# Kernel tuning notes

Hardware: AMD Instinct MI355X
Metric: run time of the kernel (lower is better)

## Reference

```python
import jax, jax.numpy as jnp
import numpy as np

B, T, H_DIM, N_HEADS, FACTOR = 1, 2048, 2048, 16, 2
KEY_DIM = H_DIM // N_HEADS          # 128
V_DIM = H_DIM * FACTOR              # 4096
HEAD_DIM = V_DIM // N_HEADS         # 256
SCALING = KEY_DIM ** -0.5
EPS = 1e-6


def rotate_every_two(x):
    x1 = x[..., ::2]
    x2 = x[..., 1::2]
    return jnp.stack([-x2, x1], axis=-1).reshape(x.shape)


def theta_shift(x, sin, cos):
    return x * cos + rotate_every_two(x) * sin


def setup_inputs() -> dict:
    key = jax.random.key(0)
    ks = jax.random.split(key, 11)
    s = 0.02  # xavier-ish init scale
    inp = {
        'hidden_states': jax.random.normal(ks[0], (B, T, H_DIM), jnp.float32),
        'Wq': jax.random.normal(ks[1], (H_DIM, H_DIM), jnp.float32) * s,
        'bq': jnp.zeros((H_DIM,), jnp.float32),
        'Wk': jax.random.normal(ks[2], (H_DIM, H_DIM), jnp.float32) * s,
        'bk': jnp.zeros((H_DIM,), jnp.float32),
        'Wv': jax.random.normal(ks[3], (H_DIM, V_DIM), jnp.float32) * s,
        'bv': jnp.zeros((V_DIM,), jnp.float32),
        'Wg': jax.random.normal(ks[4], (H_DIM, V_DIM), jnp.float32) * s,
        'bg': jnp.zeros((V_DIM,), jnp.float32),
        'Wo': jax.random.normal(ks[5], (V_DIM, H_DIM), jnp.float32) * s,
        'bo': jnp.zeros((H_DIM,), jnp.float32),
    }
    # --- RetNetRelPos (parallel mode), as in syncdoth/RetNet ---
    angle = 1.0 / (10000 ** np.linspace(0, 1, KEY_DIM // 2))
    angle = np.repeat(angle, 2)                      # [key_dim]
    index = np.arange(T)
    inp['sin'] = jnp.asarray(np.sin(index[:, None] * angle[None, :]).astype(np.float32))
    inp['cos'] = jnp.asarray(np.cos(index[:, None] * angle[None, :]).astype(np.float32))
    decay = np.log(1 - 2.0 ** (-5 - np.arange(N_HEADS, dtype=np.float64)))  # [h], negative
    diff = index[:, None] - index[None, :]           # [T,T]
    tri = diff >= 0                                  # causal mask
    expo = decay[:, None, None] * np.where(tri, diff, 0)[None]  # [h,T,T]
    mask = np.where(tri[None], np.exp(expo), 0.0)
    mask = mask / np.sqrt(mask.sum(-1, keepdims=True))
    inp['decay_mask'] = jnp.asarray(mask[None].astype(np.float32))  # [1,h,T,T]
    return inp


def _msr_forward(hidden_states, sin, cos, decay_mask,
                 Wq, bq, Wk, bk, Wv, bv, Wg, bg, Wo, bo):
    Bsz, Tlen, _ = hidden_states.shape
    q = hidden_states @ Wq + bq                      # [B,T,H]
    k = hidden_states @ Wk + bk
    v = hidden_states @ Wv + bv                      # [B,T,V_DIM]
    g = hidden_states @ Wg + bg
    # split heads -> [B,h,T,dim]
    q = q.reshape(Bsz, Tlen, N_HEADS, KEY_DIM).transpose(0, 2, 1, 3)
    k = k.reshape(Bsz, Tlen, N_HEADS, KEY_DIM).transpose(0, 2, 1, 3)
    v = v.reshape(Bsz, Tlen, N_HEADS, HEAD_DIM).transpose(0, 2, 1, 3)
    k = k * SCALING
    qr = theta_shift(q, sin, cos)                    # sin/cos broadcast over B,h
    kr = theta_shift(k, sin, cos)
    # parallel retention: QK^T scaled by decay mask, row-normalized (detached denom)
    retention = jnp.einsum('bhsk,bhtk->bhst', qr, kr) * decay_mask
    denom = jnp.clip(jnp.abs(jax.lax.stop_gradient(retention).sum(-1, keepdims=True)), 1.0, None)
    retention = retention / denom
    out = jnp.einsum('bhst,bhtd->bshd', retention, v)  # [B,T,h,head_dim]
    # group_norm: LayerNorm over head_dim, eps=1e-6, no affine
    mu = out.mean(-1, keepdims=True)
    var = out.var(-1, keepdims=True)
    normed = ((out - mu) / jnp.sqrt(var + EPS)).reshape(Bsz, Tlen, V_DIM)
    gated = jax.nn.silu(g) * normed
    return gated @ Wo + bo                           # [B,T,H]


def reference(hidden_states, sin, cos, decay_mask,
              Wq, bq, Wk, bk, Wv, bv, Wg, bg, Wo, bo):
    return _msr_forward(hidden_states, sin, cos, decay_mask,
                        Wq, bq, Wk, bk, Wv, bv, Wg, bg, Wo, bo)
```

## Files before the change

### kernel.cpp

```cpp
#include <hip/hip_runtime.h>
#include <hip/hip_bf16.h>

typedef __hip_bfloat16 bf16;
typedef __attribute__((ext_vector_type(8))) __bf16 bf16x8;
typedef __attribute__((ext_vector_type(4))) float f32x4;

constexpr int TT = 2048;
constexpr int HD = 2048;
constexpr int VD = 4096;
constexpr int KD = 128;
constexpr int NH = 16;
constexpr int DH = 256;
constexpr float K_SCALING = 0.08838834764831845f;

__device__ __forceinline__ bf16 f2bf(float x) { return __float2bfloat16(x); }
__device__ __forceinline__ unsigned short f2bfu(float x) {
    bf16 b = __float2bfloat16(x);
    return *reinterpret_cast<unsigned short*>(&b);
}
__device__ __forceinline__ float bf2f(unsigned short u) {
    unsigned int x = ((unsigned int)u) << 16;
    return __uint_as_float(x);
}

__global__ __launch_bounds__(256) void transpose_all_k(
    const float* __restrict__ Wq, const float* __restrict__ Wk,
    const float* __restrict__ Wv, const float* __restrict__ Wg,
    const float* __restrict__ Wo, bf16* __restrict__ Wcat, bf16* __restrict__ WoT,
    const float* __restrict__ hidden, bf16* __restrict__ hb)
{
    __shared__ unsigned short sT[64 * 72];
    int t2 = blockIdx.x;
    if (t2 >= 8192) {
        const int b = t2 - 8192;
        const size_t base = (size_t)b * 8192;
#pragma unroll
        for (int j = 0; j < 8; ++j) {
            const size_t i = base + j * 1024 + threadIdx.x * 4;
            float4 v = *(const float4*)(hidden + i);
            bf16 tmp[4] = {f2bf(v.x), f2bf(v.y), f2bf(v.z), f2bf(v.w)};
            *(uint2*)(hb + i) = *(const uint2*)tmp;
        }
        return;
    }
    const float* src;
    bf16* dst;
    int R, C;
    if (t2 < 1024)      { src = Wq; dst = Wcat;                     R = 2048; C = 2048; }
    else if (t2 < 2048) { src = Wk; dst = Wcat + (size_t)2048 * HD; R = 2048; C = 2048; t2 -= 1024; }
    else if (t2 < 4096) { src = Wv; dst = Wcat + (size_t)4096 * HD; R = 2048; C = 4096; t2 -= 2048; }
    else if (t2 < 6144) { src = Wg; dst = Wcat + (size_t)8192 * HD; R = 2048; C = 4096; t2 -= 4096; }
    else                { src = Wo; dst = WoT;                      R = 4096; C = 2048; t2 -= 6144; }
    const int xt = C >> 6;
    const int x0 = (t2 % xt) * 64;
    const int y0 = (t2 / xt) * 64;

    const int t = threadIdx.x;
    {
        const int r = t >> 2;
        const int c0 = (t & 3) << 4;
        const float* s = src + (size_t)(y0 + r) * C + x0 + c0;
        unsigned short e[16];
#pragma unroll
        for (int j = 0; j < 4; ++j) {
            float4 v = *(const float4*)(s + j * 4);
            e[j * 4 + 0] = f2bfu(v.x);
            e[j * 4 + 1] = f2bfu(v.y);
            e[j * 4 + 2] = f2bfu(v.z);
            e[j * 4 + 3] = f2bfu(v.w);
        }
#pragma unroll
        for (int i = 0; i < 16; ++i) {
            const int c = c0 + i;
            sT[c * 72 + (r ^ (((c >> 3) & 7) << 3))] = e[i];
        }
    }
    __syncthreads();
    {
        const int c = t >> 2;
        const int r0 = (t & 3) << 4;
        const int xs = ((c >> 3) & 7) << 3;
#pragma unroll
        for (int s2 = 0; s2 < 16; s2 += 8) {
            bf16x8 v = *(const bf16x8*)&sT[c * 72 + ((r0 + s2) ^ xs)];
            *(bf16x8*)&dst[(size_t)(x0 + c) * R + y0 + r0 + s2] = v;
        }
    }
}

__global__ __launch_bounds__(256) void transpose_bf16_k(const bf16* __restrict__ in,
                                                        bf16* __restrict__ outb) {
    __shared__ unsigned short sT[64 * 72];
    const int tid = threadIdx.x;
    const int x0 = blockIdx.x * 64;
    const int y0 = blockIdx.y * 64;
    {
        const int lt = tid >> 2;
        const int c0 = (tid & 3) << 4;
        unsigned short e[16];
        *(bf16x8*)&e[0] = *(const bf16x8*)&in[(size_t)(y0 + lt) * VD + x0 + c0];
        *(bf16x8*)&e[8] = *(const bf16x8*)&in[(size_t)(y0 + lt) * VD + x0 + c0 + 8];
#pragma unroll
        for (int i = 0; i < 16; ++i) {
            const int c = c0 + i;
            sT[c * 72 + (lt ^ (((c >> 3) & 7) << 3))] = e[i];
        }
    }
    __syncthreads();
    {
        const int c = tid >> 2;
        const int r0 = (tid & 3) << 4;
        const int xs = ((c >> 3) & 7) << 3;
#pragma unroll
        for (int s2 = 0; s2 < 16; s2 += 8) {
            bf16x8 v = *(const bf16x8*)&sT[c * 72 + ((r0 + s2) ^ xs)];
            *(bf16x8*)&outb[(size_t)(x0 + c) * TT + y0 + r0 + s2] = v;
        }
    }
}

#define GLL(gptr, lptr) __builtin_amdgcn_global_load_lds( \
    (const __attribute__((address_space(1))) void*)(gptr), \
    (__attribute__((address_space(3))) void*)(lptr), 16, 0, 0)

#define STA(bufs, u, k1) GLL(gA0 + (size_t)((u) * 64) * HD + (k1), sA + (bufs) + (u) * 4096 + tid * 8)
#define STB(bufs, u, k1) GLL(gB0 + (size_t)((u) * 64) * HD + (k1), sB + (bufs) + (u) * 4096 + tid * 8)

#define WAIT6 asm volatile("s_waitcnt vmcnt(6)" ::: "memory")
#define WAIT0V asm volatile("s_waitcnt vmcnt(0)" ::: "memory")
#define MEMF asm volatile("" ::: "memory")
#define BAR __builtin_amdgcn_s_barrier()

#define LDA(dst, cb, qm) \
    _Pragma("unroll") for (int mi = 0; mi < 4; ++mi) { \
        const int r_ = wr * 128 + (qm) * 64 + mi * 16 + lr; \
        _Pragma("unroll") for (int ks = 0; ks < 2; ++ks) \
            dst[mi][ks] = *(const bf16x8*)&sA[(cb) + r_ * 64 + (((ks * 4 + g) ^ (lr & 7)) << 3)]; \
    }

#define LDB01(dst, cb) \
    _Pragma("unroll") for (int ni = 0; ni < 2; ++ni) { \
        const int n_ = wcn * 48 + ni * 16 + lr; \
        _Pragma("unroll") for (int ks = 0; ks < 2; ++ks) \
            dst[ni][ks] = *(const bf16x8*)&sB[(cb) + n_ * 64 + (((ks * 4 + g) ^ (lr & 7)) << 3)]; \
    }

#define LDB2(dst, cb) { \
        const int n_ = wcn * 48 + 32 + lr; \
        _Pragma("unroll") for (int ks = 0; ks < 2; ++ks) \
            dst[ks] = *(const bf16x8*)&sB[(cb) + n_ * 64 + (((ks * 4 + g) ^ (lr & 7)) << 3)]; \
    }

#define Q00 __builtin_amdgcn_s_setprio(1); \
    _Pragma("unroll") for (int mi = 0; mi < 4; ++mi) \
        _Pragma("unroll") for (int ni = 0; ni < 2; ++ni) \
            _Pragma("unroll") for (int ks = 0; ks < 2; ++ks) \
                acc[mi][ni] = __builtin_amdgcn_mfma_f32_16x16x32_bf16(ra0[mi][ks], rb[ni][ks], acc[mi][ni], 0, 0, 0); \
    __builtin_amdgcn_s_setprio(0);
#define Q10 __builtin_amdgcn_s_setprio(1); \
    _Pragma("unroll") for (int mi = 0; mi < 4; ++mi) \
        _Pragma("unroll") for (int ni = 0; ni < 2; ++ni) \
            _Pragma("unroll") for (int ks = 0; ks < 2; ++ks) \
                acc[4 + mi][ni] = __builtin_amdgcn_mfma_f32_16x16x32_bf16(ra1[mi][ks], rb[ni][ks], acc[4 + mi][ni], 0, 0, 0); \
    __builtin_amdgcn_s_setprio(0);
#define Q11 __builtin_amdgcn_s_setprio(1); \
    _Pragma("unroll") for (int mi = 0; mi < 4; ++mi) \
        _Pragma("unroll") for (int ks = 0; ks < 2; ++ks) \
            acc[4 + mi][2] = __builtin_amdgcn_mfma_f32_16x16x32_bf16(ra1[mi][ks], rb2[ks], acc[4 + mi][2], 0, 0, 0); \
    __builtin_amdgcn_s_setprio(0);
#define Q01 __builtin_amdgcn_s_setprio(1); \
    _Pragma("unroll") for (int mi = 0; mi < 4; ++mi) \
        _Pragma("unroll") for (int ks = 0; ks < 2; ++ks) \
            acc[mi][2] = __builtin_amdgcn_mfma_f32_16x16x32_bf16(ra0[mi][ks], rb2[ks], acc[mi][2], 0, 0, 0); \
    __builtin_amdgcn_s_setprio(0);

__global__ __launch_bounds__(512, 2) void gemm_qkvg_k(
    const bf16* __restrict__ Ag, const bf16* __restrict__ Bg,
    const float* __restrict__ bq, const float* __restrict__ bk,
    const float* __restrict__ bvp, const float* __restrict__ bg,
    const float* __restrict__ sinT, const float* __restrict__ cosT,
    bf16* __restrict__ qr, bf16* __restrict__ kr,
    bf16* __restrict__ vtmp, bf16* __restrict__ sg)
{
    __shared__ unsigned short sA[2 * 256 * 64];
    __shared__ unsigned short sB[2 * 192 * 64];
    constexpr int BUFA = 16384, BUFB = 12288;

    const int tid = threadIdx.x;
    const int lane = tid & 63;
    const int w = tid >> 6;
    const int wr = w >> 2;
    const int wcn = w & 3;
    const int lr = lane & 15;
    const int g = lane >> 4;

    const int flat = blockIdx.x;
    const int swz = (flat & 7) * 64 + (flat >> 3);
    const int brow = (swz & 7) * 256;
    const int bcol = (swz >> 3) * 192;

    const bf16* gA0 = Ag + (size_t)(brow + (tid >> 3)) * HD + (((tid & 7) ^ ((tid >> 3) & 7)) << 3);
    const bf16* gB0 = Bg + (size_t)(bcol + (tid >> 3)) * HD + (((tid & 7) ^ ((tid >> 3) & 7)) << 3);

    f32x4 acc[8][3] = {};
    bf16x8 ra0[4][2], ra1[4][2], rb[2][2], rb2[2];

    STA(0, 0, 0); STA(0, 1, 0); STA(0, 2, 0); STA(0, 3, 0);
    STB(0, 0, 0); STB(0, 1, 0); STB(0, 2, 0);
    STA(BUFA, 0, 64); STA(BUFA, 1, 64); STA(BUFA, 2, 64); STA(BUFA, 3, 64);
    STB(BUFB, 0, 64); STB(BUFB, 1, 64);
    WAIT6; MEMF; BAR;

    for (int I = 0; I < 15; ++I) {
        const int kB1 = I * 128 + 64;
        const int kN2 = I * 128 + 128;
        const int kN3 = I * 128 + 192;
        LDA(ra0, 0, 0) LDB01(rb, 0)
        STB(BUFB, 2, kB1);
        MEMF; BAR; Q00 BAR;
        LDA(ra1, 0, 1)
        STA(0, 0, kN2); STA(0, 2, kN2);
        MEMF; BAR; Q10 BAR;
        LDB2(rb2, 0)
        STA(0, 1, kN2); STA(0, 3, kN2);
        MEMF; BAR; Q11 BAR;
        STB(0, 0, kN2); STB(0, 1, kN2);
        WAIT6; MEMF; BAR; Q01 BAR;
        LDA(ra0, BUFA, 0) LDB01(rb, BUFB)
        STB(0, 2, kN2);
        MEMF; BAR; Q00 BAR;
        LDA(ra1, BUFA, 1)
        STA(BUFA, 0, kN3); STA(BUFA, 2, kN3);
        MEMF; BAR; Q10 BAR;
        LDB2(rb2, BUFB)
        STA(BUFA, 1, kN3); STA(BUFA, 3, kN3);
        MEMF; BAR; Q11 BAR;
        STB(BUFB, 0, kN3); STB(BUFB, 1, kN3);
        WAIT6; MEMF; BAR; Q01 BAR;
    }
    {
        LDA(ra0, 0, 0) LDB01(rb, 0)
        STB(BUFB, 2, 1984);
        MEMF; BAR; Q00 BAR;
        LDA(ra1, 0, 1)
        MEMF; BAR; Q10 BAR;
        LDB2(rb2, 0)
        MEMF; BAR; Q11 BAR;
        WAIT0V; MEMF; BAR; Q01 BAR;
        LDA(ra0, BUFA, 0) LDB01(rb, BUFB)
        Q00
        LDA(ra1, BUFA, 1)
        Q10
        LDB2(rb2, BUFB)
        Q11
        Q01
    }

#pragma unroll
    for (int M = 0; M < 8; ++M) {
        const int row = brow + wr * 128 + (M >> 2) * 64 + (M & 3) * 16 + g * 4;
#pragma unroll
        for (int f = 0; f < 3; ++f) {
            const int colg = bcol + wcn * 48 + f * 16 + lr;
            if (colg < 4096) {
                const bool isK = (colg >= 2048);
                const int col = colg - (isK ? 2048 : 0);
                const float bvv = (isK ? bk : bq)[col];
                const float scale = isK ? K_SCALING : 1.f;
                bf16* outb = isK ? kr : qr;
                const int d = col & (KD - 1);
#pragma unroll
                for (int r = 0; r < 4; ++r) {
                    float v = (acc[M][f][r] + bvv) * scale;
                    float o = __shfl_xor(v, 1);
                    float rot = (col & 1) ? o : -o;
                    outb[(size_t)(row + r) * HD + col] =
                        f2bf(v * cosT[(row + r) * KD + d] + rot * sinT[(row + r) * KD + d]);
                }
            } else if (colg < 8192) {
                const int col = colg - 4096;
                const float bvv = bvp[col];
#pragma unroll
                for (int r = 0; r < 4; ++r)
                    vtmp[(size_t)(row + r) * VD + col] = f2bf(acc[M][f][r] + bvv);
            } else {
                const int col = colg - 8192;
                const float bvv = bg[col];
#pragma unroll
                for (int r = 0; r < 4; ++r) {
                    float v = acc[M][f][r] + bvv;
                    sg[(size_t)(row + r) * VD + col] = f2bf(v / (1.f + __expf(-v)));
                }
            }
        }
    }
}

__global__ __launch_bounds__(256) void gemm_out_k(
    const bf16* __restrict__ Ag, const bf16* __restrict__ Bg,
    float* __restrict__ outp)
{
    __shared__ unsigned short sOA[128 * 32];
    __shared__ unsigned short sOB[128 * 32];

    const int flat = blockIdx.x;
    const int swz = (flat & 7) * 32 + (flat >> 3);
    const int brow = (swz & 15) * 128;
    const int bcol = (swz >> 4) * 128;
    const int kbase = blockIdx.y * 2048;

    const int tid = threadIdx.x;
    const int lane = tid & 63;
    const int wid = tid >> 6;
    const int wr = wid >> 1, wc = wid & 1;

    f32x4 acc[4][4] = {};

    const int lr = lane & 15;
    const int lk = (lane >> 4) << 3;
    const int r0 = tid >> 2;
    const int c0 = (tid & 3) << 3;
    const int ldsw = (tid & 192) << 3;

    for (int k0 = kbase; k0 < kbase + 2048; k0 += 32) {
        const bf16* gA = Ag + (size_t)(brow + r0) * VD + k0 + c0;
        const bf16* gB = Bg + (size_t)(bcol + r0) * VD + k0 + c0;
        GLL(gA, sOA + ldsw);
        GLL(gB, sOB + ldsw);
        GLL(gA + 64 * VD, sOA + 2048 + ldsw);
        GLL(gB + 64 * VD, sOB + 2048 + ldsw);
        __syncthreads();

        bf16x8 af[4], bv[4];
#pragma unroll
        for (int mi = 0; mi < 4; ++mi)
            af[mi] = *(const bf16x8*)&sOA[(wr * 64 + mi * 16 + lr) * 32 + lk];
#pragma unroll
        for (int ni = 0; ni < 4; ++ni)
            bv[ni] = *(const bf16x8*)&sOB[(wc * 64 + ni * 16 + lr) * 32 + lk];
#pragma unroll
        for (int mi = 0; mi < 4; ++mi)
#pragma unroll
            for (int ni = 0; ni < 4; ++ni)
                acc[mi][ni] = __builtin_amdgcn_mfma_f32_16x16x32_bf16(af[mi], bv[ni], acc[mi][ni], 0, 0, 0);
        __syncthreads();
    }

    float* op = outp + (size_t)blockIdx.y * TT * HD;
    const int row0 = brow + wr * 64 + ((lane >> 4) << 2);
    const int col0 = bcol + wc * 64 + lr;
#pragma unroll
    for (int mi = 0; mi < 4; ++mi) {
#pragma unroll
        for (int ni = 0; ni < 4; ++ni) {
            const int col = col0 + ni * 16;
#pragma unroll
            for (int r = 0; r < 4; ++r) {
                const int row = row0 + mi * 16 + r;
                op[(size_t)row * HD + col] = acc[mi][ni][r];
            }
        }
    }
}

__global__ __launch_bounds__(256) void combine_out_k(const float* __restrict__ outp,
                                                     const float* __restrict__ bias,
                                                     float* __restrict__ out) {
    const size_t i = ((size_t)blockIdx.x * 256 + threadIdx.x) * 4;
    float4 a = *(const float4*)(outp + i);
    float4 b = *(const float4*)(outp + (size_t)TT * HD + i);
    float4 bi = *(const float4*)(bias + (i & (HD - 1)));
    float4 o;
    o.x = a.x + b.x + bi.x;
    o.y = a.y + b.y + bi.y;
    o.z = a.z + b.z + bi.z;
    o.w = a.w + b.w + bi.w;
    *(float4*)(out + i) = o;
}

__global__ __launch_bounds__(512) void retention_fused_k(
    const bf16* __restrict__ qr, const bf16* __restrict__ kr,
    const bf16* __restrict__ vT,
    bf16* __restrict__ po0, bf16* __restrict__ po1,
    float* __restrict__ pr0, float* __restrict__ pr1)
{
    __shared__ unsigned short P_lds[2 * 128 * 128];
    __shared__ float rsum_lds[4][128];

    const int tid = threadIdx.x;
    const int lane = tid & 63;
    const int wid = tid >> 6;
    const int wr64 = (wid >> 2) * 64;
    const int wc = wid & 3;
    const int lr = lane & 15;
    const int g = lane >> 4;
    const int lk = g << 3;
    const int pidx = blockIdx.x;
    const int parity = blockIdx.y;
    const int h = blockIdx.z;

    const float decay = logf(1.f - exp2f(-5.f - (float)h));
    bf16* __restrict__ po = parity ? po1 : po0;
    float* __restrict__ pr = parity ? pr1 : pr0;

    const int swzA = (lr & 7) << 3;

    const float bfac0 = __expf(decay * (float)(-(wc * 32 + lr)));
    const float bfac1 = __expf(decay * (float)(-(wc * 32 + 16 + lr)));
    const float astep = __expf(decay * -256.f);

    for (int sec = 0; sec < 2; ++sec) {
        const int qb = sec ? (15 - pidx) : pidx;
        const int qrow0 = qb * 128;

        bf16x8 af[4][4];
#pragma unroll
        for (int mi = 0; mi < 4; ++mi)
#pragma unroll
            for (int ks = 0; ks < 4; ++ks)
                af[mi][ks] = *(const bf16x8*)&qr[(size_t)(qrow0 + wr64 + mi * 16 + lr) * HD +
                                                 h * KD + ks * 32 + lk];

        f32x4 acc_o[4][4] = {};
        float rs[4][4] = {};
        float aexp[4][4];
#pragma unroll
        for (int mi = 0; mi < 4; ++mi)
#pragma unroll
            for (int r = 0; r < 4; ++r) {
                const int row_l = wr64 + mi * 16 + g * 4 + r;
                aexp[mi][r] = __expf(decay * (float)(qrow0 + row_l - parity * 128));
            }

        int pb = 0;
        for (int tb = parity; tb <= qb; tb += 2) {
            const int t0 = tb * 128;

            f32x4 acc_p[4][2] = {};
#pragma unroll
            for (int ks = 0; ks < 4; ++ks) {
                const bf16x8 b0 = *(const bf16x8*)&kr[(size_t)(t0 + wc * 32 + lr) * HD +
                                                      h * KD + ks * 32 + lk];
                const bf16x8 b1 = *(const bf16x8*)&kr[(size_t)(t0 + wc * 32 + 16 + lr) * HD +
                                                      h * KD + ks * 32 + lk];
#pragma unroll
                for (int mi = 0; mi < 4; ++mi) {
                    acc_p[mi][0] = __builtin_amdgcn_mfma_f32_16x16x32_bf16(af[mi][ks], b0, acc_p[mi][0], 0, 0, 0);
                    acc_p[mi][1] = __builtin_amdgcn_mfma_f32_16x16x32_bf16(af[mi][ks], b1, acc_p[mi][1], 0, 0, 0);
                }
            }

#pragma unroll
            for (int mi = 0; mi < 4; ++mi) {
#pragma unroll
                for (int r = 0; r < 4; ++r) {
                    const int rl = g * 4 + r;
                    const int row_l = wr64 + mi * 16 + rl;
                    const int srel = qrow0 + row_l - t0;
                    const float a = aexp[mi][r];
                    const float p0 = (wc * 32 + lr <= srel) ? acc_p[mi][0][r] * a * bfac0 : 0.f;
                    const float p1 = (wc * 32 + 16 + lr <= srel) ? acc_p[mi][1][r] * a * bfac1 : 0.f;
                    const int sw = (rl & 7) << 3;
                    P_lds[pb + row_l * 128 + ((wc * 32 + lr) ^ sw)] = f2bfu(p0);
                    P_lds[pb + row_l * 128 + ((wc * 32 + 16 + lr) ^ sw)] = f2bfu(p1);
                    rs[mi][r] += p0 + p1;
                    aexp[mi][r] = a * astep;
                }
            }
            __syncthreads();

#pragma unroll
            for (int ks2 = 0; ks2 < 4; ++ks2) {
                bf16x8 a2[4], b2[4];
#pragma unroll
                for (int mi = 0; mi < 4; ++mi)
                    a2[mi] = *(const bf16x8*)&P_lds[pb + (wr64 + mi * 16 + lr) * 128 +
                                                    ((ks2 * 32 + lk) ^ swzA)];
#pragma unroll
                for (int ni = 0; ni < 4; ++ni)
                    b2[ni] = *(const bf16x8*)&vT[(size_t)(h * DH + wc * 64 + ni * 16 + lr) * TT +
                                                 t0 + ks2 * 32 + lk];
#pragma unroll
                for (int mi = 0; mi < 4; ++mi)
#pragma unroll
                    for (int ni = 0; ni < 4; ++ni)
                        acc_o[mi][ni] = __builtin_amdgcn_mfma_f32_16x16x32_bf16(a2[mi], b2[ni], acc_o[mi][ni], 0, 0, 0);
            }
            pb ^= 16384;
        }

#pragma unroll
        for (int mi = 0; mi < 4; ++mi)
#pragma unroll
            for (int r = 0; r < 4; ++r) {
                float v = rs[mi][r];
                v += __shfl_xor(v, 1);
                v += __shfl_xor(v, 2);
                v += __shfl_xor(v, 4);
                v += __shfl_xor(v, 8);
                if (lr == 0) rsum_lds[wc][wr64 + mi * 16 + g * 4 + r] = v;
            }
        __syncthreads();
        if (tid < 128)
            pr[(size_t)h * TT + qrow0 + tid] =
                rsum_lds[0][tid] + rsum_lds[1][tid] + rsum_lds[2][tid] + rsum_lds[3][tid];

#pragma unroll
        for (int mi = 0; mi < 4; ++mi)
#pragma unroll
            for (int ni = 0; ni < 4; ++ni)
#pragma unroll
                for (int r = 0; r < 4; ++r) {
                    const int row_l = wr64 + mi * 16 + g * 4 + r;
                    const int col = wc * 64 + ni * 16 + lr;
                    po[(size_t)(qrow0 + row_l) * VD + h * DH + col] = f2bf(acc_o[mi][ni][r]);
                }
        __syncthreads();
    }
}

__global__ __launch_bounds__(256) void ln_gate_k(const bf16* __restrict__ po0,
                                                 const bf16* __restrict__ po1,
                                                 const float* __restrict__ pr0,
                                                 const float* __restrict__ pr1,
                                                 const bf16* __restrict__ sg,
                                                 bf16* __restrict__ gated) {
    const int tid = threadIdx.x;
    const int lane = tid & 63;
    const size_t ridx = (size_t)blockIdx.x * 4 + (tid >> 6);
    const int h = (int)(ridx & 15);
    const int s = (int)(ridx >> 4);

    const float decay = logf(1.f - exp2f(-5.f - (float)h));
    const float Sm = -expm1f(decay * (float)(s + 1)) * exp2f(5.f + (float)h);
    const float norm = rsqrtf(Sm);
    const float raw = pr0[(size_t)h * TT + s] + pr1[(size_t)h * TT + s];
    const float scale = norm / fmaxf(1.f, fabsf(raw * norm));

    unsigned short ua[4], ub[4];
    *(uint2*)ua = *(const uint2*)(po0 + ridx * 256 + lane * 4);
    *(uint2*)ub = *(const uint2*)(po1 + ridx * 256 + lane * 4);
    float vv[4];
#pragma unroll
    for (int i = 0; i < 4; ++i)
        vv[i] = (bf2f(ua[i]) + bf2f(ub[i])) * scale;
    float sm = vv[0] + vv[1] + vv[2] + vv[3];
    float sq = vv[0] * vv[0] + vv[1] * vv[1] + vv[2] * vv[2] + vv[3] * vv[3];
#pragma unroll
    for (int o = 1; o < 64; o <<= 1) {
        sm += __shfl_xor(sm, o);
        sq += __shfl_xor(sq, o);
    }
    const float mu = sm * (1.f / 256.f);
    const float var = sq * (1.f / 256.f) - mu * mu;
    const float rstd = rsqrtf(var + 1e-6f);
    const bf16* sgp = sg + ridx * 256 + lane * 4;
    bf16* gp = gated + ridx * 256 + lane * 4;
    bf16 ob[4];
#pragma unroll
    for (int i = 0; i < 4; ++i)
        ob[i] = f2bf((vv[i] - mu) * rstd * __bfloat162float(sgp[i]));
    *(uint2*)gp = *(const uint2*)ob;
}

extern "C" void kernel_launch(void* const* d_in, const int* in_sizes, int n_in,
                              void* d_out, int out_size, void* d_ws, size_t ws_size,
                              hipStream_t stream) {
    const float* hidden = (const float*)d_in[0];
    const float* Wq = (const float*)d_in[1];
    const float* bq = (const float*)d_in[2];
    const float* Wk = (const float*)d_in[3];
    const float* bk = (const float*)d_in[4];
    const float* Wv = (const float*)d_in[5];
    const float* bvp = (const float*)d_in[6];
    const float* Wg = (const float*)d_in[7];
    const float* bg = (const float*)d_in[8];
    const float* Wo = (const float*)d_in[9];
    const float* bo = (const float*)d_in[10];
    const float* sinT = (const float*)d_in[11];
    const float* cosT = (const float*)d_in[12];
    float* out = (float*)d_out;

    char* p = (char*)d_ws;
    bf16* hb = (bf16*)p;    p += (size_t)TT * HD * 2;
    bf16* Wcat = (bf16*)p;  p += (size_t)(HD + HD + VD + VD) * HD * 2;
    bf16* WoT = (bf16*)p;   p += (size_t)HD * VD * 2;
    bf16* qr = (bf16*)p;    p += (size_t)TT * HD * 2;
    bf16* kr = (bf16*)p;    p += (size_t)TT * HD * 2;
    bf16* vtmp = (bf16*)p;  p += (size_t)TT * VD * 2;
    bf16* vT = (bf16*)p;    p += (size_t)VD * TT * 2;
    bf16* sg = (bf16*)p;    p += (size_t)TT * VD * 2;
    bf16* po0 = (bf16*)p;   p += (size_t)TT * VD * 2;
    bf16* po1 = (bf16*)p;   p += (size_t)TT * VD * 2;
    float* pr0 = (float*)p; p += (size_t)NH * TT * 4;
    float* pr1 = (float*)p; p += (size_t)NH * TT * 4;
    bf16* gated = (bf16*)p; p += (size_t)TT * VD * 2;
    float* outp = (float*)p; p += (size_t)2 * TT * HD * 4;

    transpose_all_k<<<8704, 256, 0, stream>>>(Wq, Wk, Wv, Wg, Wo, Wcat, WoT, hidden, hb);

    gemm_qkvg_k<<<512, 512, 0, stream>>>(hb, Wcat, bq, bk, bvp, bg, sinT, cosT,
                                         qr, kr, vtmp, sg);
    transpose_bf16_k<<<dim3(VD / 64, TT / 64), 256, 0, stream>>>(vtmp, vT);

    retention_fused_k<<<dim3(8, 2, NH), 512, 0, stream>>>(qr, kr, vT, po0, po1, pr0, pr1);

    ln_gate_k<<<TT * NH / 4, 256, 0, stream>>>(po0, po1, pr0, pr1, sg, gated);
    gemm_out_k<<<dim3(256, 2), 256, 0, stream>>>(gated, WoT, outp);
    combine_out_k<<<TT * HD / 1024, 256, 0, stream>>>(outp, bo, out);
}
```

Before: 333.9 us.

## Write V transposed from QKVG GEMM epilogue and atomically reduce split-K output

The QKVG GEMM epilogue now writes V directly in transposed layout with packed 4-element stores, which removes the separate transpose kernel and its intermediate buffer. The output GEMM's two split-K halves now atomically add into a zeroed output, with bias added by one half, which replaces the partial-sum buffer and the combine kernel. This saves two launches and the round trips through intermediate buffers. In exchange it adds a memset, scalar float atomics on every output element, a non-deterministic summation order, and strided writes into the transposed V.

```diff
diff --git a/kernel.cpp b/kernel.cpp
--- a/kernel.cpp
+++ b/kernel.cpp
@@ -84,37 +84,6 @@
         for (int s2 = 0; s2 < 16; s2 += 8) {
             bf16x8 v = *(const bf16x8*)&sT[c * 72 + ((r0 + s2) ^ xs)];
             *(bf16x8*)&dst[(size_t)(x0 + c) * R + y0 + r0 + s2] = v;
-        }
-    }
-}
-
-__global__ __launch_bounds__(256) void transpose_bf16_k(const bf16* __restrict__ in,
-                                                        bf16* __restrict__ outb) {
-    __shared__ unsigned short sT[64 * 72];
-    const int tid = threadIdx.x;
-    const int x0 = blockIdx.x * 64;
-    const int y0 = blockIdx.y * 64;
-    {
-        const int lt = tid >> 2;
-        const int c0 = (tid & 3) << 4;
-        unsigned short e[16];
-        *(bf16x8*)&e[0] = *(const bf16x8*)&in[(size_t)(y0 + lt) * VD + x0 + c0];
-        *(bf16x8*)&e[8] = *(const bf16x8*)&in[(size_t)(y0 + lt) * VD + x0 + c0 + 8];
-#pragma unroll
-        for (int i = 0; i < 16; ++i) {
-            const int c = c0 + i;
-            sT[c * 72 + (lt ^ (((c >> 3) & 7) << 3))] = e[i];
-        }
-    }
-    __syncthreads();
-    {
-        const int c = tid >> 2;
-        const int r0 = (tid & 3) << 4;
-        const int xs = ((c >> 3) & 7) << 3;
-#pragma unroll
-        for (int s2 = 0; s2 < 16; s2 += 8) {
-            bf16x8 v = *(const bf16x8*)&sT[c * 72 + ((r0 + s2) ^ xs)];
-            *(bf16x8*)&outb[(size_t)(x0 + c) * TT + y0 + r0 + s2] = v;
         }
     }
 }
@@ -180,7 +149,7 @@
     const float* __restrict__ bvp, const float* __restrict__ bg,
     const float* __restrict__ sinT, const float* __restrict__ cosT,
     bf16* __restrict__ qr, bf16* __restrict__ kr,
-    bf16* __restrict__ vtmp, bf16* __restrict__ sg)
+    bf16* __restrict__ vT, bf16* __restrict__ sg)
 {
     __shared__ unsigned short sA[2 * 256 * 64];
     __shared__ unsigned short sB[2 * 192 * 64];
@@ -280,9 +249,11 @@
             } else if (colg < 8192) {
                 const int col = colg - 4096;
                 const float bvv = bvp[col];
+                bf16 tmp[4];
 #pragma unroll
                 for (int r = 0; r < 4; ++r)
-                    vtmp[(size_t)(row + r) * VD + col] = f2bf(acc[M][f][r] + bvv);
+                    tmp[r] = f2bf(acc[M][f][r] + bvv);
+                *(uint2*)&vT[(size_t)col * TT + row] = *(const uint2*)tmp;
             } else {
                 const int col = colg - 8192;
                 const float bvv = bg[col];
@@ -298,7 +269,7 @@
 
 __global__ __launch_bounds__(256) void gemm_out_k(
     const bf16* __restrict__ Ag, const bf16* __restrict__ Bg,
-    float* __restrict__ outp)
+    const float* __restrict__ bias, float* __restrict__ out)
 {
     __shared__ unsigned short sOA[128 * 32];
     __shared__ unsigned short sOB[128 * 32];
@@ -346,7 +317,6 @@
         __syncthreads();
     }
 
-    float* op = outp + (size_t)blockIdx.y * TT * HD;
     const int row0 = brow + wr * 64 + ((lane >> 4) << 2);
     const int col0 = bcol + wc * 64 + lr;
 #pragma unroll
@@ -354,28 +324,14 @@
 #pragma unroll
         for (int ni = 0; ni < 4; ++ni) {
             const int col = col0 + ni * 16;
+            const float bvv = (blockIdx.y == 0) ? bias[col] : 0.f;
 #pragma unroll
             for (int r = 0; r < 4; ++r) {
                 const int row = row0 + mi * 16 + r;
-                op[(size_t)row * HD + col] = acc[mi][ni][r];
-            }
-        }
-    }
-}
-
-__global__ __launch_bounds__(256) void combine_out_k(const float* __restrict__ outp,
-                                                     const float* __restrict__ bias,
-                                                     float* __restrict__ out) {
-    const size_t i = ((size_t)blockIdx.x * 256 + threadIdx.x) * 4;
-    float4 a = *(const float4*)(outp + i);
-    float4 b = *(const float4*)(outp + (size_t)TT * HD + i);
-    float4 bi = *(const float4*)(bias + (i & (HD - 1)));
-    float4 o;
-    o.x = a.x + b.x + bi.x;
-    o.y = a.y + b.y + bi.y;
-    o.z = a.z + b.z + bi.z;
-    o.w = a.w + b.w + bi.w;
-    *(float4*)(out + i) = o;
+                atomicAdd(&out[(size_t)row * HD + col], acc[mi][ni][r] + bvv);
+            }
+        }
+    }
 }
 
 __global__ __launch_bounds__(512) void retention_fused_k(
@@ -587,7 +543,6 @@
     bf16* WoT = (bf16*)p;   p += (size_t)HD * VD * 2;
     bf16* qr = (bf16*)p;    p += (size_t)TT * HD * 2;
     bf16* kr = (bf16*)p;    p += (size_t)TT * HD * 2;
-    bf16* vtmp = (bf16*)p;  p += (size_t)TT * VD * 2;
     bf16* vT = (bf16*)p;    p += (size_t)VD * TT * 2;
     bf16* sg = (bf16*)p;    p += (size_t)TT * VD * 2;
     bf16* po0 = (bf16*)p;   p += (size_t)TT * VD * 2;
@@ -595,17 +550,16 @@
     float* pr0 = (float*)p; p += (size_t)NH * TT * 4;
     float* pr1 = (float*)p; p += (size_t)NH * TT * 4;
     bf16* gated = (bf16*)p; p += (size_t)TT * VD * 2;
-    float* outp = (float*)p; p += (size_t)2 * TT * HD * 4;
+
+    hipMemsetAsync(out, 0, (size_t)TT * HD * 4, stream);
 
     transpose_all_k<<<8704, 256, 0, stream>>>(Wq, Wk, Wv, Wg, Wo, Wcat, WoT, hidden, hb);
 
     gemm_qkvg_k<<<512, 512, 0, stream>>>(hb, Wcat, bq, bk, bvp, bg, sinT, cosT,
-                                         qr, kr, vtmp, sg);
-    transpose_bf16_k<<<dim3(VD / 64, TT / 64), 256, 0, stream>>>(vtmp, vT);
+                                         qr, kr, vT, sg);
 
     retention_fused_k<<<dim3(8, 2, NH), 512, 0, stream>>>(qr, kr, vT, po0, po1, pr0, pr1);
 
     ln_gate_k<<<TT * NH / 4, 256, 0, stream>>>(po0, po1, pr0, pr1, sg, gated);
-    gemm_out_k<<<dim3(256, 2), 256, 0, stream>>>(gated, WoT, outp);
-    combine_out_k<<<TT * HD / 1024, 256, 0, stream>>>(outp, bo, out);
-}
+    gemm_out_k<<<dim3(256, 2), 256, 0, stream>>>(gated, WoT, bo, out);
+}
```

Measured after the change: 336.3 us. No clear change (+0.7%).
